# Performance work log

Measured on AMD Instinct MI355X. Metric: run time of the kernel, lower is better.

## Reference

```python
import jax, jax.numpy as jnp
import numpy as np
import math

BATCH, L, H, P = 8, 2048, 1024, 512
DT_MIN, DT_MAX = 1e-3, 1e-1
STEP_RESCALE = 1.0


def setup_inputs() -> dict:
    key = jax.random.key(0)
    ks = jax.random.split(key, 8)
    signal = jax.random.normal(ks[0], (BATCH, L, H), dtype=jnp.float32)
    prev_state = jnp.zeros((BATCH, P), dtype=jnp.float32)
    # S5-style init: Lambda_re < 0, Lambda_im = pi * k
    Lambda_re = -0.5 * jnp.ones((P,), dtype=jnp.float32)
    Lambda_im = math.pi * jnp.arange(P, dtype=jnp.float32)
    # B stored as real (P,H,2) -> complex B_tilde; lecun scale 1/sqrt(H)
    B = jax.random.normal(ks[1], (P, H, 2), dtype=jnp.float32) / math.sqrt(H)
    # C stored as real (H,P,2) -> complex C_tilde; lecun scale 1/sqrt(P)
    C = jax.random.normal(ks[2], (H, P, 2), dtype=jnp.float32) / math.sqrt(P)
    D = jax.random.normal(ks[3], (H,), dtype=jnp.float32)
    u = jax.random.uniform(ks[4], (P, 1), dtype=jnp.float32)
    log_step = u * (math.log(DT_MAX) - math.log(DT_MIN)) + math.log(DT_MIN)
    return {"signal": signal, "prev_state": prev_state,
            "Lambda_re": Lambda_re, "Lambda_im": Lambda_im,
            "B": B, "C": C, "D": D, "log_step": log_step}


def _binop(qi, qj):
    # parallel-scan combine for diagonal linear recurrence x_t = A_t x_{t-1} + b_t
    A_i, b_i = qi
    A_j, b_j = qj
    return (A_j * A_i, b_j + A_j * b_i)


def reference(signal, prev_state, Lambda_re, Lambda_im, B, C, D, log_step):
    Lambda = Lambda_re + 1j * Lambda_im                      # (P,) complex
    B_tilde = B[..., 0] + 1j * B[..., 1]                     # (P,H)
    C_tilde = C[..., 0] + 1j * C[..., 1]                     # (H,P)
    step = STEP_RESCALE * jnp.exp(log_step[:, 0])            # (P,)
    # zero-order hold discretization
    Lambda_bar = jnp.exp(Lambda * step)                      # (P,)
    B_bar = ((Lambda_bar - 1.0) / Lambda)[:, None] * B_tilde # (P,H)
    # Bu elements: (BATCH, L, P) complex
    Bu = jnp.einsum('blh,ph->blp', signal.astype(B_bar.dtype), B_bar)
    # A elements: Lambda_bar tiled over time; first element carries prev_state
    A_first = (Lambda_bar[None, :] * prev_state.astype(Lambda_bar.dtype))[:, None, :]
    A_rest = jnp.broadcast_to(Lambda_bar, (signal.shape[0], signal.shape[1] - 1, Lambda_bar.shape[0]))
    A = jnp.concatenate([A_first, A_rest], axis=1)           # (BATCH, L, P)
    _, xs = jax.lax.associative_scan(_binop, (A, Bu), axis=1)  # xs: (BATCH, L, P)
    # conj_sym=True -> 2 * Re(C_tilde @ x), plus feedthrough D*u
    y = 2.0 * jnp.einsum('blp,hp->blh', xs, C_tilde).real + D * signal
    state = xs[:, -1]                                        # (BATCH, P) complex
    return y, state
```

## Files before the change

kernel.cpp:

```cpp
#include <hip/hip_runtime.h>
#include <math.h>

#define L_SEQ   2048
#define BATCH_N 8
#define H_DIM   1024
#define P_DIM   512
#define M_DIM   (BATCH_N * L_SEQ)
#define N2      1024
#define NC      32
#define T_CHUNK 64

typedef __attribute__((ext_vector_type(8))) __bf16 bf16x8;
typedef __attribute__((ext_vector_type(4))) float f32x4;

__device__ __forceinline__ unsigned f2bf_bits(float f) {
    unsigned u = __builtin_bit_cast(unsigned, f);
    return (u + 0x7fffu + ((u >> 16) & 1u)) >> 16;
}
__device__ __forceinline__ float bf_lo(unsigned v) {
    return __builtin_bit_cast(float, v << 16);
}
__device__ __forceinline__ float bf_hi(unsigned v) {
    return __builtin_bit_cast(float, v & 0xffff0000u);
}
__device__ __forceinline__ float bf2f(unsigned short u) {
    return __builtin_bit_cast(float, (unsigned)u << 16);
}

#define ASYNC_COPY16(gsrc, ldst)                                            \
    __builtin_amdgcn_global_load_lds(                                       \
        (__attribute__((address_space(1))) void*)(gsrc),                    \
        (__attribute__((address_space(3))) void*)(ldst), 16, 0, 0)

__global__ void setup_lam(const float* __restrict__ Lre_in,
                          const float* __restrict__ Lim_in,
                          const float* __restrict__ log_step,
                          float* __restrict__ lam) {
    int p = blockIdx.x * blockDim.x + threadIdx.x;
    if (p >= P_DIM) return;
    float step = expf(log_step[p]);
    float c = Lre_in[p];
    float d = Lim_in[p];
    float mag = expf(c * step);
    float ang = d * step;
    float lr = mag * cosf(ang);
    float li = mag * sinf(ang);
    float a = lr - 1.0f, b = li;
    float inv = 1.0f / (c * c + d * d);
    lam[p]             = lr;
    lam[P_DIM + p]     = li;
    lam[2 * P_DIM + p] = (a * c + b * d) * inv;
    lam[3 * P_DIM + p] = (b * c - a * d) * inv;
}

__global__ void build_W(const float* __restrict__ B,
                        const float* __restrict__ C,
                        const float* __restrict__ lam,
                        unsigned short* __restrict__ W1,
                        unsigned short* __restrict__ W2) {
    int idx = blockIdx.x * blockDim.x + threadIdx.x;
    if (idx < P_DIM * H_DIM) {
        int p = idx >> 10;
        int h = idx & (H_DIM - 1);
        float bre = B[(size_t)idx * 2];
        float bim = B[(size_t)idx * 2 + 1];
        float gre = lam[2 * P_DIM + p];
        float gim = lam[3 * P_DIM + p];
        W1[(size_t)p * H_DIM + h]           = (unsigned short)f2bf_bits(gre * bre - gim * bim);
        W1[(size_t)(P_DIM + p) * H_DIM + h] = (unsigned short)f2bf_bits(gre * bim + gim * bre);
    } else {
        int j = idx - P_DIM * H_DIM;
        int h = j >> 9;
        int p = j & (P_DIM - 1);
        float cre = C[(size_t)j * 2];
        float cim = C[(size_t)j * 2 + 1];
        W2[(size_t)h * N2 + p]         = (unsigned short)f2bf_bits( 2.0f * cre);
        W2[(size_t)h * N2 + P_DIM + p] = (unsigned short)f2bf_bits(-2.0f * cim);
    }
}

__global__ void convert_sig(const float* __restrict__ in,
                            unsigned short* __restrict__ out) {
    size_t i = ((size_t)blockIdx.x * 256 + threadIdx.x) * 4;
    float4 v = *(const float4*)(in + i);
    ushort4 o;
    o.x = (unsigned short)f2bf_bits(v.x);
    o.y = (unsigned short)f2bf_bits(v.y);
    o.z = (unsigned short)f2bf_bits(v.z);
    o.w = (unsigned short)f2bf_bits(v.w);
    *(ushort4*)(out + i) = o;
}

template <int MODE>
__global__ __launch_bounds__(512, 2) void gemm_mfma(
    const unsigned short* __restrict__ A,
    const unsigned short* __restrict__ W,
    void* __restrict__ Out, int K,
    const float* __restrict__ Dvec, const unsigned short* __restrict__ SigBf)
{
    __shared__ unsigned short smem[65536];

    const int tid  = threadIdx.x;
    const int lane = tid & 63;
    const int wid  = tid >> 6;
    const int wm   = wid >> 2;
    const int wn   = wid & 3;

    const int id  = blockIdx.x;
    const int wg  = (id & 7) * 32 + (id >> 3);
    const int m0  = (wg >> 2) * 256;
    const int n0  = (wg & 3) * 256;

    const int fr  = lane & 15;
    const int fq  = lane >> 4;
    const int ks0 = ((fq + (fr >> 1)) & 7) * 8;
    const int ks1 = ks0 ^ 32;
    const int qg  = ((tid & 7) - ((tid >> 4) & 7)) & 7;

    const int NKT = K >> 6;

    auto STAGE = [&](const unsigned short* __restrict__ Mat, int mn0,
                     int half, int kt, int bofs) {
        const unsigned short* s = Mat
            + (size_t)(mn0 + half * 128 + (tid >> 3)) * K + (kt << 6) + qg * 8;
        unsigned short* d = smem + (kt & 1) * 32768 + bofs
            + (half * 1024 + wid * 64) * 8;
        ASYNC_COPY16(s, d);
        ASYNC_COPY16(s + (size_t)64 * K, d + 4096);
    };

    f32x4 acc[8][4] = {};

    STAGE(A, m0, 0, 0, 0);      STAGE(A, m0, 1, 0, 0);
    STAGE(W, n0, 0, 0, 16384);  STAGE(W, n0, 1, 0, 16384);
    STAGE(W, n0, 0, 1, 16384);  STAGE(A, m0, 0, 1, 0);
    asm volatile("s_waitcnt vmcnt(4)" ::: "memory");
    __builtin_amdgcn_s_barrier();

    #pragma unroll 1
    for (int kt = 0; kt < NKT; ++kt) {
        const unsigned short* Ab =
            smem + (kt & 1) * 32768 + (wm * 128 + fr) * 64;
        const unsigned short* Wb =
            smem + (kt & 1) * 32768 + 16384 + (wn * 64 + fr) * 64;
        bf16x8 af[4][2], w0[2][2], w1[2][2];

        #pragma unroll
        for (int mi = 0; mi < 4; ++mi) {
            af[mi][0] = *(const bf16x8*)&Ab[mi * 1024 + ks0];
            af[mi][1] = *(const bf16x8*)&Ab[mi * 1024 + ks1];
        }
        #pragma unroll
        for (int ni = 0; ni < 2; ++ni) {
            w0[ni][0] = *(const bf16x8*)&Wb[ni * 1024 + ks0];
            w0[ni][1] = *(const bf16x8*)&Wb[ni * 1024 + ks1];
        }
        if (kt + 1 < NKT) {
            STAGE(A, m0, 1, kt + 1, 0);
            STAGE(W, n0, 1, kt + 1, 16384);
        }
        __builtin_amdgcn_s_barrier();
        asm volatile("s_waitcnt lgkmcnt(0)" ::: "memory");
        __builtin_amdgcn_sched_barrier(0);
        __builtin_amdgcn_s_setprio(1);
        #pragma unroll
        for (int mi = 0; mi < 4; ++mi)
            #pragma unroll
            for (int ni = 0; ni < 2; ++ni) {
                acc[mi][ni] = __builtin_amdgcn_mfma_f32_16x16x32_bf16(
                    af[mi][0], w0[ni][0], acc[mi][ni], 0, 0, 0);
                acc[mi][ni] = __builtin_amdgcn_mfma_f32_16x16x32_bf16(
                    af[mi][1], w0[ni][1], acc[mi][ni], 0, 0, 0);
            }
        __builtin_amdgcn_s_setprio(0);
        __builtin_amdgcn_s_barrier();

        #pragma unroll
        for (int ni = 0; ni < 2; ++ni) {
            w1[ni][0] = *(const bf16x8*)&Wb[(2 + ni) * 1024 + ks0];
            w1[ni][1] = *(const bf16x8*)&Wb[(2 + ni) * 1024 + ks1];
        }
        __builtin_amdgcn_s_barrier();
        asm volatile("s_waitcnt lgkmcnt(0)" ::: "memory");
        __builtin_amdgcn_sched_barrier(0);
        __builtin_amdgcn_s_setprio(1);
        #pragma unroll
        for (int mi = 0; mi < 4; ++mi)
            #pragma unroll
            for (int ni = 0; ni < 2; ++ni) {
                acc[mi][2 + ni] = __builtin_amdgcn_mfma_f32_16x16x32_bf16(
                    af[mi][0], w1[ni][0], acc[mi][2 + ni], 0, 0, 0);
                acc[mi][2 + ni] = __builtin_amdgcn_mfma_f32_16x16x32_bf16(
                    af[mi][1], w1[ni][1], acc[mi][2 + ni], 0, 0, 0);
            }
        __builtin_amdgcn_s_setprio(0);
        __builtin_amdgcn_s_barrier();

        #pragma unroll
        for (int mi = 0; mi < 4; ++mi) {
            af[mi][0] = *(const bf16x8*)&Ab[4096 + mi * 1024 + ks0];
            af[mi][1] = *(const bf16x8*)&Ab[4096 + mi * 1024 + ks1];
        }
        if (kt + 2 < NKT)
            STAGE(W, n0, 0, kt + 2, 16384);
        __builtin_amdgcn_s_barrier();
        asm volatile("s_waitcnt lgkmcnt(0)" ::: "memory");
        __builtin_amdgcn_sched_barrier(0);
        __builtin_amdgcn_s_setprio(1);
        #pragma unroll
        for (int mi = 0; mi < 4; ++mi)
            #pragma unroll
            for (int ni = 0; ni < 2; ++ni) {
                acc[4 + mi][ni] = __builtin_amdgcn_mfma_f32_16x16x32_bf16(
                    af[mi][0], w0[ni][0], acc[4 + mi][ni], 0, 0, 0);
                acc[4 + mi][ni] = __builtin_amdgcn_mfma_f32_16x16x32_bf16(
                    af[mi][1], w0[ni][1], acc[4 + mi][ni], 0, 0, 0);
            }
        __builtin_amdgcn_s_setprio(0);
        __builtin_amdgcn_s_barrier();

        if (kt + 2 < NKT)
            STAGE(A, m0, 0, kt + 2, 0);
        __builtin_amdgcn_s_barrier();
        __builtin_amdgcn_s_setprio(1);
        #pragma unroll
        for (int mi = 0; mi < 4; ++mi)
            #pragma unroll
            for (int ni = 0; ni < 2; ++ni) {
                acc[4 + mi][2 + ni] = __builtin_amdgcn_mfma_f32_16x16x32_bf16(
                    af[mi][0], w1[ni][0], acc[4 + mi][2 + ni], 0, 0, 0);
                acc[4 + mi][2 + ni] = __builtin_amdgcn_mfma_f32_16x16x32_bf16(
                    af[mi][1], w1[ni][1], acc[4 + mi][2 + ni], 0, 0, 0);
            }
        __builtin_amdgcn_s_setprio(0);
        if (kt == NKT - 2)
            asm volatile("s_waitcnt vmcnt(0)" ::: "memory");
        else
            asm volatile("s_waitcnt vmcnt(4)" ::: "memory");
        __builtin_amdgcn_s_barrier();
    }

    if (MODE == 0) {
        unsigned short* T = smem;
        #pragma unroll
        for (int h = 0; h < 2; ++h) {
            __syncthreads();
            if (wm == h) {
                #pragma unroll
                for (int mi = 0; mi < 8; ++mi)
                    #pragma unroll
                    for (int ni = 0; ni < 4; ++ni)
                        #pragma unroll
                        for (int r = 0; r < 4; ++r) {
                            int lrow = mi * 16 + fq * 4 + r;
                            int lcol = wn * 64 + ni * 16 + fr;
                            T[lrow * 264 + lcol] =
                                (unsigned short)f2bf_bits(acc[mi][ni][r]);
                        }
            }
            __syncthreads();
            #pragma unroll
            for (int jj = 0; jj < 8; ++jj) {
                int chunk = jj * 512 + tid;
                int row = chunk >> 5;
                int co  = (chunk & 31) * 8;
                *(ulonglong2*)((unsigned short*)Out +
                    (size_t)(m0 + h * 128 + row) * 1024 + n0 + co) =
                    *(const ulonglong2*)&T[row * 264 + co];
            }
        }
    } else {
        float Dl[4];
        #pragma unroll
        for (int ni = 0; ni < 4; ++ni)
            Dl[ni] = Dvec[n0 + wn * 64 + ni * 16 + fr];
        #pragma unroll
        for (int mi = 0; mi < 8; ++mi) {
            #pragma unroll
            for (int ni = 0; ni < 4; ++ni) {
                #pragma unroll
                for (int r = 0; r < 4; ++r) {
                    int row = m0 + wm * 128 + mi * 16 + fq * 4 + r;
                    int col = n0 + wn * 64 + ni * 16 + fr;
                    float v = acc[mi][ni][r];
                    v = fmaf(Dl[ni], bf2f(SigBf[(size_t)row * 1024 + col]), v);
                    ((float*)Out)[(size_t)row * 1024 + col] = v;
                }
            }
        }
    }
}

__global__ __launch_bounds__(256) void scan_sums(
    const unsigned short* __restrict__ Bu, const float* __restrict__ lam,
    float* __restrict__ S)
{
    int b = blockIdx.x, c = blockIdx.y, t = threadIdx.x;
    int p0 = 2 * t, p1 = 2 * t + 1;
    float lr0 = lam[p0], li0 = lam[P_DIM + p0];
    float lr1 = lam[p1], li1 = lam[P_DIM + p1];
    const unsigned* base =
        (const unsigned*)(Bu + ((size_t)b * L_SEQ + (size_t)c * T_CHUNK) * N2);
    float xr0 = 0, xi0 = 0, xr1 = 0, xi1 = 0;
    for (int j0 = 0; j0 < T_CHUNK; j0 += 8) {
        unsigned R[8], I[8];
        #pragma unroll
        for (int j = 0; j < 8; ++j) {
            R[j] = base[(size_t)(j0 + j) * 512 + t];
            I[j] = base[(size_t)(j0 + j) * 512 + 256 + t];
        }
        #pragma unroll
        for (int j = 0; j < 8; ++j) {
            float nr0 = fmaf(lr0, xr0, fmaf(-li0, xi0, bf_lo(R[j])));
            float ni0 = fmaf(lr0, xi0, fmaf( li0, xr0, bf_lo(I[j])));
            float nr1 = fmaf(lr1, xr1, fmaf(-li1, xi1, bf_hi(R[j])));
            float ni1 = fmaf(lr1, xi1, fmaf( li1, xr1, bf_hi(I[j])));
            xr0 = nr0; xi0 = ni0; xr1 = nr1; xi1 = ni1;
        }
    }
    float* Sb = S + ((size_t)(b * NC + c) * 2) * P_DIM;
    Sb[p0] = xr0; Sb[p1] = xr1;
    Sb[P_DIM + p0] = xi0; Sb[P_DIM + p1] = xi1;
}

__global__ __launch_bounds__(512) void scan_carry(
    const float* __restrict__ S, const float* __restrict__ lam,
    float* __restrict__ CIN)
{
    int b = blockIdx.x, p = threadIdx.x;
    float lr = lam[p], li = lam[P_DIM + p];
    float pr = lr, pi = li;
    #pragma unroll
    for (int i = 0; i < 6; ++i) {
        float nr = pr * pr - pi * pi;
        float ni = 2.0f * pr * pi;
        pr = nr; pi = ni;
    }
    float cr = 0, ci = 0;
    for (int c = 0; c < NC; ++c) {
        float* Cb = CIN + ((size_t)(b * NC + c) * 2) * P_DIM;
        Cb[p] = cr; Cb[P_DIM + p] = ci;
        const float* Sb = S + ((size_t)(b * NC + c) * 2) * P_DIM;
        float sr = Sb[p], si = Sb[P_DIM + p];
        float nr = fmaf(pr, cr, fmaf(-pi, ci, sr));
        float ni = fmaf(pr, ci, fmaf( pi, cr, si));
        cr = nr; ci = ni;
    }
}

__global__ __launch_bounds__(256) void scan_apply(
    unsigned short* __restrict__ Bu, const float* __restrict__ lam,
    const float* __restrict__ CIN, float* __restrict__ out_state,
    int interleaved)
{
    int b = blockIdx.x, c = blockIdx.y, t = threadIdx.x;
    int p0 = 2 * t, p1 = 2 * t + 1;
    float lr0 = lam[p0], li0 = lam[P_DIM + p0];
    float lr1 = lam[p1], li1 = lam[P_DIM + p1];
    const float* Cb = CIN + ((size_t)(b * NC + c) * 2) * P_DIM;
    float xr0 = Cb[p0], xi0 = Cb[P_DIM + p0];
    float xr1 = Cb[p1], xi1 = Cb[P_DIM + p1];
    unsigned* base =
        (unsigned*)(Bu + ((size_t)b * L_SEQ + (size_t)c * T_CHUNK) * N2);
    for (int j0 = 0; j0 < T_CHUNK; j0 += 8) {
        unsigned R[8], I[8];
        #pragma unroll
        for (int j = 0; j < 8; ++j) {
            R[j] = base[(size_t)(j0 + j) * 512 + t];
            I[j] = base[(size_t)(j0 + j) * 512 + 256 + t];
        }
        #pragma unroll
        for (int j = 0; j < 8; ++j) {
            float nr0 = fmaf(lr0, xr0, fmaf(-li0, xi0, bf_lo(R[j])));
            float ni0 = fmaf(lr0, xi0, fmaf( li0, xr0, bf_lo(I[j])));
            float nr1 = fmaf(lr1, xr1, fmaf(-li1, xi1, bf_hi(R[j])));
            float ni1 = fmaf(lr1, xi1, fmaf( li1, xr1, bf_hi(I[j])));
            xr0 = nr0; xi0 = ni0; xr1 = nr1; xi1 = ni1;
            R[j] = f2bf_bits(nr0) | (f2bf_bits(nr1) << 16);
            I[j] = f2bf_bits(ni0) | (f2bf_bits(ni1) << 16);
        }
        #pragma unroll
        for (int j = 0; j < 8; ++j) {
            base[(size_t)(j0 + j) * 512 + t]       = R[j];
            base[(size_t)(j0 + j) * 512 + 256 + t] = I[j];
        }
    }
    if (c == NC - 1) {
        if (interleaved) {
            out_state[((size_t)b * P_DIM + p0) * 2]     = xr0;
            out_state[((size_t)b * P_DIM + p0) * 2 + 1] = xi0;
            out_state[((size_t)b * P_DIM + p1) * 2]     = xr1;
            out_state[((size_t)b * P_DIM + p1) * 2 + 1] = xi1;
        } else {
            out_state[(size_t)b * P_DIM + p0] = xr0;
            out_state[(size_t)b * P_DIM + p1] = xr1;
        }
    }
}

extern "C" void kernel_launch(void* const* d_in, const int* in_sizes, int n_in,
                              void* d_out, int out_size, void* d_ws, size_t ws_size,
                              hipStream_t stream)
{
    const float* signal   = (const float*)d_in[0];
    const float* Lre      = (const float*)d_in[2];
    const float* Lim      = (const float*)d_in[3];
    const float* B        = (const float*)d_in[4];
    const float* C        = (const float*)d_in[5];
    const float* Dv       = (const float*)d_in[6];
    const float* log_step = (const float*)d_in[7];

    char* ws = (char*)d_ws;
    unsigned short* sigbf = (unsigned short*)ws;
    unsigned short* Bubf  = (unsigned short*)(ws + 33554432);
    unsigned short* W1bf  = (unsigned short*)(ws + 67108864);
    unsigned short* W2bf  = (unsigned short*)(ws + 69206016);
    float*          lam   = (float*)(ws + 71303168);
    float*          S     = (float*)(ws + 71311360);
    float*          CIN   = (float*)(ws + 71835648);
    size_t need = 72359936;
    if (ws_size < need) return;

    float* y_out = (float*)d_out;
    float* state_out = y_out + (size_t)M_DIM * H_DIM;
    int interleaved = (out_size - M_DIM * H_DIM) >= 2 * BATCH_N * P_DIM;

    setup_lam<<<dim3(2), dim3(256), 0, stream>>>(Lre, Lim, log_step, lam);
    build_W<<<dim3((2 * P_DIM * H_DIM) / 256), dim3(256), 0, stream>>>(
        B, C, lam, W1bf, W2bf);
    convert_sig<<<dim3((M_DIM * H_DIM) / 1024), dim3(256), 0, stream>>>(signal, sigbf);

    gemm_mfma<0><<<dim3(256), dim3(512), 0, stream>>>(
        sigbf, W1bf, Bubf, H_DIM, nullptr, nullptr);

    scan_sums<<<dim3(BATCH_N, NC), dim3(256), 0, stream>>>(Bubf, lam, S);
    scan_carry<<<dim3(BATCH_N), dim3(512), 0, stream>>>(S, lam, CIN);
    scan_apply<<<dim3(BATCH_N, NC), dim3(256), 0, stream>>>(
        Bubf, lam, CIN, state_out, interleaved);

    gemm_mfma<1><<<dim3(256), dim3(512), 0, stream>>>(
        Bubf, W2bf, y_out, N2, Dv, sigbf);
}
```

Measured before the change: 241.9 us.

## Load all W fragments up front and reschedule async stages in GEMM mainloop

Result: no change. 242.9 us (+0.4%).

```diff
diff --git a/kernel.cpp b/kernel.cpp
--- a/kernel.cpp
+++ b/kernel.cpp
@@ -131,10 +131,11 @@
 
     f32x4 acc[8][4] = {};
 
+    STAGE(W, n0, 0, 0, 16384);  STAGE(W, n0, 1, 0, 16384);
     STAGE(A, m0, 0, 0, 0);      STAGE(A, m0, 1, 0, 0);
-    STAGE(W, n0, 0, 0, 16384);  STAGE(W, n0, 1, 0, 16384);
-    STAGE(W, n0, 0, 1, 16384);  STAGE(A, m0, 0, 1, 0);
-    asm volatile("s_waitcnt vmcnt(4)" ::: "memory");
+    STAGE(W, n0, 0, 1, 16384);  STAGE(W, n0, 1, 1, 16384);
+    STAGE(A, m0, 0, 1, 0);
+    asm volatile("s_waitcnt vmcnt(6)" ::: "memory");
     __builtin_amdgcn_s_barrier();
 
     #pragma unroll 1
@@ -143,7 +144,7 @@
             smem + (kt & 1) * 32768 + (wm * 128 + fr) * 64;
         const unsigned short* Wb =
             smem + (kt & 1) * 32768 + 16384 + (wn * 64 + fr) * 64;
-        bf16x8 af[4][2], w0[2][2], w1[2][2];
+        bf16x8 af[4][2], wf[4][2];
 
         #pragma unroll
         for (int mi = 0; mi < 4; ++mi) {
@@ -151,14 +152,12 @@
             af[mi][1] = *(const bf16x8*)&Ab[mi * 1024 + ks1];
         }
         #pragma unroll
-        for (int ni = 0; ni < 2; ++ni) {
-            w0[ni][0] = *(const bf16x8*)&Wb[ni * 1024 + ks0];
-            w0[ni][1] = *(const bf16x8*)&Wb[ni * 1024 + ks1];
-        }
-        if (kt + 1 < NKT) {
+        for (int ni = 0; ni < 4; ++ni) {
+            wf[ni][0] = *(const bf16x8*)&Wb[ni * 1024 + ks0];
+            wf[ni][1] = *(const bf16x8*)&Wb[ni * 1024 + ks1];
+        }
+        if (kt + 1 < NKT)
             STAGE(A, m0, 1, kt + 1, 0);
-            STAGE(W, n0, 1, kt + 1, 16384);
-        }
         __builtin_amdgcn_s_barrier();
         asm volatile("s_waitcnt lgkmcnt(0)" ::: "memory");
         __builtin_amdgcn_sched_barrier(0);
@@ -168,18 +167,36 @@
             #pragma unroll
             for (int ni = 0; ni < 2; ++ni) {
                 acc[mi][ni] = __builtin_amdgcn_mfma_f32_16x16x32_bf16(
-                    af[mi][0], w0[ni][0], acc[mi][ni], 0, 0, 0);
+                    af[mi][0], wf[ni][0], acc[mi][ni], 0, 0, 0);
                 acc[mi][ni] = __builtin_amdgcn_mfma_f32_16x16x32_bf16(
-                    af[mi][1], w0[ni][1], acc[mi][ni], 0, 0, 0);
+                    af[mi][1], wf[ni][1], acc[mi][ni], 0, 0, 0);
             }
         __builtin_amdgcn_s_setprio(0);
         __builtin_amdgcn_s_barrier();
 
-        #pragma unroll
-        for (int ni = 0; ni < 2; ++ni) {
-            w1[ni][0] = *(const bf16x8*)&Wb[(2 + ni) * 1024 + ks0];
-            w1[ni][1] = *(const bf16x8*)&Wb[(2 + ni) * 1024 + ks1];
-        }
+        if (kt + 2 < NKT)
+            STAGE(W, n0, 0, kt + 2, 16384);
+        __builtin_amdgcn_s_barrier();
+        __builtin_amdgcn_s_setprio(1);
+        #pragma unroll
+        for (int mi = 0; mi < 4; ++mi)
+            #pragma unroll
+            for (int ni = 0; ni < 2; ++ni) {
+                acc[mi][2 + ni] = __builtin_amdgcn_mfma_f32_16x16x32_bf16(
+                    af[mi][0], wf[2 + ni][0], acc[mi][2 + ni], 0, 0, 0);
+                acc[mi][2 + ni] = __builtin_amdgcn_mfma_f32_16x16x32_bf16(
+                    af[mi][1], wf[2 + ni][1], acc[mi][2 + ni], 0, 0, 0);
+            }
+        __builtin_amdgcn_s_setprio(0);
+        __builtin_amdgcn_s_barrier();
+
+        #pragma unroll
+        for (int mi = 0; mi < 4; ++mi) {
+            af[mi][0] = *(const bf16x8*)&Ab[4096 + mi * 1024 + ks0];
+            af[mi][1] = *(const bf16x8*)&Ab[4096 + mi * 1024 + ks1];
+        }
+        if (kt + 2 < NKT)
+            STAGE(W, n0, 1, kt + 2, 16384);
         __builtin_amdgcn_s_barrier();
         asm volatile("s_waitcnt lgkmcnt(0)" ::: "memory");
         __builtin_amdgcn_sched_barrier(0);
@@ -188,33 +205,10 @@
         for (int mi = 0; mi < 4; ++mi)
             #pragma unroll
             for (int ni = 0; ni < 2; ++ni) {
-                acc[mi][2 + ni] = __builtin_amdgcn_mfma_f32_16x16x32_bf16(
-                    af[mi][0], w1[ni][0], acc[mi][2 + ni], 0, 0, 0);
-                acc[mi][2 + ni] = __builtin_amdgcn_mfma_f32_16x16x32_bf16(
-                    af[mi][1], w1[ni][1], acc[mi][2 + ni], 0, 0, 0);
-            }
-        __builtin_amdgcn_s_setprio(0);
-        __builtin_amdgcn_s_barrier();
-
-        #pragma unroll
-        for (int mi = 0; mi < 4; ++mi) {
-            af[mi][0] = *(const bf16x8*)&Ab[4096 + mi * 1024 + ks0];
-            af[mi][1] = *(const bf16x8*)&Ab[4096 + mi * 1024 + ks1];
-        }
-        if (kt + 2 < NKT)
-            STAGE(W, n0, 0, kt + 2, 16384);
-        __builtin_amdgcn_s_barrier();
-        asm volatile("s_waitcnt lgkmcnt(0)" ::: "memory");
-        __builtin_amdgcn_sched_barrier(0);
-        __builtin_amdgcn_s_setprio(1);
-        #pragma unroll
-        for (int mi = 0; mi < 4; ++mi)
-            #pragma unroll
-            for (int ni = 0; ni < 2; ++ni) {
                 acc[4 + mi][ni] = __builtin_amdgcn_mfma_f32_16x16x32_bf16(
-                    af[mi][0], w0[ni][0], acc[4 + mi][ni], 0, 0, 0);
+                    af[mi][0], wf[ni][0], acc[4 + mi][ni], 0, 0, 0);
                 acc[4 + mi][ni] = __builtin_amdgcn_mfma_f32_16x16x32_bf16(
-                    af[mi][1], w0[ni][1], acc[4 + mi][ni], 0, 0, 0);
+                    af[mi][1], wf[ni][1], acc[4 + mi][ni], 0, 0, 0);
             }
         __builtin_amdgcn_s_setprio(0);
         __builtin_amdgcn_s_barrier();
@@ -228,15 +222,15 @@
             #pragma unroll
             for (int ni = 0; ni < 2; ++ni) {
                 acc[4 + mi][2 + ni] = __builtin_amdgcn_mfma_f32_16x16x32_bf16(
-                    af[mi][0], w1[ni][0], acc[4 + mi][2 + ni], 0, 0, 0);
+                    af[mi][0], wf[2 + ni][0], acc[4 + mi][2 + ni], 0, 0, 0);
                 acc[4 + mi][2 + ni] = __builtin_amdgcn_mfma_f32_16x16x32_bf16(
-                    af[mi][1], w1[ni][1], acc[4 + mi][2 + ni], 0, 0, 0);
+                    af[mi][1], wf[2 + ni][1], acc[4 + mi][2 + ni], 0, 0, 0);
             }
         __builtin_amdgcn_s_setprio(0);
-        if (kt == NKT - 2)
+        if (kt >= NKT - 2)
             asm volatile("s_waitcnt vmcnt(0)" ::: "memory");
         else
-            asm volatile("s_waitcnt vmcnt(4)" ::: "memory");
+            asm volatile("s_waitcnt vmcnt(6)" ::: "memory");
         __builtin_amdgcn_s_barrier();
     }
 
```
